# Kernel optimization log

Measured on AMD Instinct MI355X. Metric: run time of the kernel, lower is better.

## Reference

```python
import jax, jax.numpy as jnp
import numpy as np

N_NODES = 100000

def prelu(x, alpha):
    return jnp.where(x >= 0, x, alpha * x)

def setup_inputs() -> dict:
    key = jax.random.key(0)
    ks = jax.random.split(key, 8)
    N, E, D = N_NODES, 1600000, 128
    AX = jax.random.normal(ks[0], (N, D), dtype=jnp.float32)
    A_row = jax.random.randint(ks[1], (E,), 0, N, dtype=jnp.int32)
    A_col = jax.random.randint(ks[2], (E,), 0, N, dtype=jnp.int32)
    A_val = jax.random.uniform(ks[3], (E,), dtype=jnp.float32)
    # Xavier-uniform linear weights, zero bias (as in module init)
    lim = float(np.sqrt(6.0 / (D + D)))
    Wr_w = jax.random.uniform(ks[4], (D, D), minval=-lim, maxval=lim, dtype=jnp.float32)
    W_w = jax.random.uniform(ks[5], (D, D), minval=-lim, maxval=lim, dtype=jnp.float32)
    Wr_b = jnp.zeros((D,), dtype=jnp.float32)
    W_b = jnp.zeros((D,), dtype=jnp.float32)
    g_alpha = jnp.full((1,), 0.25, dtype=jnp.float32)    # PReLU default init
    act_alpha = jnp.full((1,), 0.25, dtype=jnp.float32)
    return {"AX": AX, "A_row": A_row, "A_col": A_col, "A_val": A_val,
            "Wr_w": Wr_w, "Wr_b": Wr_b, "W_w": W_w, "W_b": W_b,
            "g_alpha": g_alpha, "act_alpha": act_alpha}

def reference(AX, A_row, A_col, A_val, Wr_w, Wr_b, W_w, W_b, g_alpha, act_alpha):
    # h = g(Wr @ AX)  : [N, H]
    h = prelu(AX @ Wr_w.T + Wr_b, g_alpha)
    # SpMM: temp[i] = sum_{(i,j) in E} A_val * h[j]
    msgs = A_val[:, None] * h[A_col]                       # [E, H] gather
    temp = jax.ops.segment_sum(msgs, A_row, num_segments=N_NODES)
    # act(W @ temp), unsqueeze batch dim
    out = prelu(temp @ W_w.T + W_b, act_alpha)
    return out[None, :, :]
```

## Files before the change

kernel.cpp:

```cpp
#include <hip/hip_runtime.h>
#include <stdint.h>


typedef _Float16 half8 __attribute__((ext_vector_type(8)));
typedef _Float16 half4 __attribute__((ext_vector_type(4)));
typedef _Float16 half2v __attribute__((ext_vector_type(2)));
typedef float floatx4 __attribute__((ext_vector_type(4)));

#define LDK 136
#define SHIFT 5
#define NBMAX 3200
#define NBLK 256
#define SCT 1024
#define CAP 1024

__global__ __launch_bounds__(256, 3)
void gemm_hist(const float* __restrict__ X, const float* __restrict__ Wr,
               const float* __restrict__ bias, const float* __restrict__ alpha_p,
               _Float16* __restrict__ out, int N,
               const int* __restrict__ rows, int* __restrict__ hist_g,
               int E, int chunk, int NB,
               const float* __restrict__ W, _Float16* __restrict__ W16)
{
    __shared__ _Float16 Ws[128 * LDK];
    const int tid = threadIdx.x;

    if (blockIdx.x < NBLK) {
        const int hb = blockIdx.x;
        int* lh = (int*)Ws;
        if (hb == 0) {
#pragma unroll
            for (int j = 0; j < 64; ++j)
                W16[tid + j * 256] = (_Float16)W[tid + j * 256];
        }
        for (int i = tid; i < NB; i += 256) lh[i] = 0;
        __syncthreads();
        int s = hb * chunk, e = min(E, s + chunk);
        for (int i = s + tid; i < e; i += 256)
            atomicAdd(&lh[rows[i] >> SHIFT], 1);
        __syncthreads();
        for (int b = tid; b < NB; b += 256)
            hist_g[b * NBLK + hb] = lh[b];
        return;
    }

    const int bm  = (blockIdx.x - NBLK) * 128;
    const float alpha = *alpha_p;
    const int wave = tid >> 6;
    const int lane = tid & 63;
    const int l15  = lane & 15;
    const int quad = lane >> 4;

    half8 a[2][4];
#pragma unroll
    for (int mt = 0; mt < 2; ++mt) {
        const int xrow = bm + wave * 32 + mt * 16 + l15;
        const float* xp = X + (size_t)xrow * 128 + quad * 8;
        const bool ok = xrow < N;
#pragma unroll
        for (int k = 0; k < 4; ++k) {
            half8 hv = {};
            if (ok) {
                float4 f0 = *(const float4*)(xp + k * 32);
                float4 f1 = *(const float4*)(xp + k * 32 + 4);
                hv[0] = (_Float16)f0.x; hv[1] = (_Float16)f0.y;
                hv[2] = (_Float16)f0.z; hv[3] = (_Float16)f0.w;
                hv[4] = (_Float16)f1.x; hv[5] = (_Float16)f1.y;
                hv[6] = (_Float16)f1.z; hv[7] = (_Float16)f1.w;
            }
            a[mt][k] = hv;
        }
    }

#pragma unroll
    for (int i = 0; i < 16; ++i) {
        int c   = tid + i * 256;
        int row = c >> 5;
        int coff = (c & 31) * 4;
        float4 f = *(const float4*)(Wr + row * 128 + coff);
        half4 hv = { (_Float16)f.x, (_Float16)f.y, (_Float16)f.z, (_Float16)f.w };
        *(half4*)(&Ws[row * LDK + coff]) = hv;
    }
    __syncthreads();

    floatx4 acc[2][8] = {};
#pragma unroll
    for (int k = 0; k < 4; ++k) {
        const int k0 = k * 32;
        half8 b[8];
#pragma unroll
        for (int n = 0; n < 8; ++n)
            b[n] = *(const half8*)(&Ws[(n * 16 + l15) * LDK + k0 + quad * 8]);
#pragma unroll
        for (int n = 0; n < 8; ++n) {
            acc[0][n] = __builtin_amdgcn_mfma_f32_16x16x32_f16(a[0][k], b[n], acc[0][n], 0, 0, 0);
            acc[1][n] = __builtin_amdgcn_mfma_f32_16x16x32_f16(a[1][k], b[n], acc[1][n], 0, 0, 0);
        }
    }

#pragma unroll
    for (int mt = 0; mt < 2; ++mt) {
#pragma unroll
        for (int n = 0; n < 8; ++n) {
#pragma unroll
            for (int r = 0; r < 4; ++r) {
                int row = bm + wave * 32 + mt * 16 + quad * 4 + r;
                int col = n * 16 + l15;
                if (row < N) {
                    float v = acc[mt][n][r] + bias[col];
                    v = (v >= 0.f) ? v : alpha * v;
                    out[(size_t)row * 128 + col] = (_Float16)v;
                }
            }
        }
    }
}

__global__ __launch_bounds__(NBLK)
void bucket_scan1(int* __restrict__ hist_g, int* __restrict__ tot)
{
    __shared__ int sd[NBLK];
    int b = blockIdx.x, t = threadIdx.x;
    int v = hist_g[b * NBLK + t];
    sd[t] = v;
    __syncthreads();
    for (int off = 1; off < NBLK; off <<= 1) {
        int x = (t >= off) ? sd[t - off] : 0;
        __syncthreads();
        sd[t] += x;
        __syncthreads();
    }
    hist_g[b * NBLK + t] = sd[t] - v;
    if (t == NBLK - 1) tot[b] = sd[t];
}

__global__ __launch_bounds__(SCT)
void bucket_scatter(const int* __restrict__ rows, const int* __restrict__ cols,
                    const float* __restrict__ vals, const int* __restrict__ tot,
                    const int* __restrict__ hist_g, uint2* __restrict__ edges,
                    int* __restrict__ bkt_ptr, int E, int chunk, int NB)
{
    __shared__ int sd[SCT];
    __shared__ int cur[NBMAX];
    const int t = threadIdx.x, blk = blockIdx.x;

    int v[4]; int s = 0;
#pragma unroll
    for (int j = 0; j < 4; ++j) {
        int idx = t * 4 + j;
        v[j] = (idx < NB) ? tot[idx] : 0;
        s += v[j];
    }
    sd[t] = s;
    __syncthreads();
    for (int off = 1; off < SCT; off <<= 1) {
        int x = (t >= off) ? sd[t - off] : 0;
        __syncthreads();
        sd[t] += x;
        __syncthreads();
    }
    int base = (t == 0) ? 0 : sd[t - 1];
#pragma unroll
    for (int j = 0; j < 4; ++j) {
        int idx = t * 4 + j;
        if (idx < NB) {
            cur[idx] = base + hist_g[idx * NBLK + blk];
            if (blk == 0) bkt_ptr[idx] = base;
            base += v[j];
        }
    }
    if (blk == 0 && t == 0) bkt_ptr[NB] = E;
    __syncthreads();

    int s0 = blk * chunk, e0 = min(E, s0 + chunk);
    for (int i = s0 + t; i < e0; i += SCT) {
        int r = rows[i];
        int b = r >> SHIFT;
        uint2 ed;
        ed.x = (unsigned)cols[i] | ((unsigned)(r & 31) << 20);
        ed.y = __float_as_uint(vals[i]);
        int p = atomicAdd(&cur[b], 1);
        edges[p] = ed;
    }
}

__global__ __launch_bounds__(256, 8)
void spmm_fused(const int* __restrict__ bkt_ptr, const uint2* __restrict__ edges,
                const _Float16* __restrict__ h, const _Float16* __restrict__ W16,
                const float* __restrict__ bias, const float* __restrict__ alpha_p,
                float* __restrict__ out, int N)
{
    __shared__ uint2 eS[CAP];
    __shared__ _Float16 T[32 * LDK];
    __shared__ int bins[32], startS[33];

    const int tid  = threadIdx.x;
    const int wave = tid >> 6;
    const int lane = tid & 63;
    const int b    = blockIdx.x;
    const int s0   = bkt_ptr[b], e0 = bkt_ptr[b + 1];

    float acc[8][2] = {};

    for (int base = s0; base < e0; base += CAP) {
        const int n = min(CAP, e0 - base);
        if (tid < 32) bins[tid] = 0;
        __syncthreads();
        uint2 q[4];
#pragma unroll
        for (int u = 0; u < 4; ++u) {
            int i = tid + u * 256;
            if (i < n) {
                q[u] = edges[base + i];
                atomicAdd(&bins[q[u].x >> 20], 1);
            }
        }
        __syncthreads();
        if (tid < 32) {
            int x = bins[tid];
#pragma unroll
            for (int off = 1; off < 32; off <<= 1) {
                int y = __shfl_up(x, off);
                if (tid >= off) x += y;
            }
            startS[tid + 1] = x;
            if (tid == 0) startS[0] = 0;
            bins[tid] = x - bins[tid];
        }
        __syncthreads();
#pragma unroll
        for (int u = 0; u < 4; ++u) {
            int i = tid + u * 256;
            if (i < n) {
                int p = atomicAdd(&bins[q[u].x >> 20], 1);
                eS[p] = q[u];
            }
        }
        __syncthreads();

#pragma unroll
        for (int j = 0; j < 8; ++j) {
            int r  = wave * 8 + j;
            int rs = startS[r], re = startS[r + 1];
            float a0r = acc[j][0], a1r = acc[j][1];
            int i = rs;
            for (; i + 7 < re; i += 8) {
                uint2 q0 = eS[i],     q1 = eS[i + 1], q2 = eS[i + 2], q3 = eS[i + 3];
                uint2 q4 = eS[i + 4], q5 = eS[i + 5], q6 = eS[i + 6], q7 = eS[i + 7];
                half2v v0 = *(const half2v*)(h + (size_t)(q0.x & 0xFFFFF) * 128 + lane * 2);
                half2v v1 = *(const half2v*)(h + (size_t)(q1.x & 0xFFFFF) * 128 + lane * 2);
                half2v v2 = *(const half2v*)(h + (size_t)(q2.x & 0xFFFFF) * 128 + lane * 2);
                half2v v3 = *(const half2v*)(h + (size_t)(q3.x & 0xFFFFF) * 128 + lane * 2);
                half2v v4 = *(const half2v*)(h + (size_t)(q4.x & 0xFFFFF) * 128 + lane * 2);
                half2v v5 = *(const half2v*)(h + (size_t)(q5.x & 0xFFFFF) * 128 + lane * 2);
                half2v v6 = *(const half2v*)(h + (size_t)(q6.x & 0xFFFFF) * 128 + lane * 2);
                half2v v7 = *(const half2v*)(h + (size_t)(q7.x & 0xFFFFF) * 128 + lane * 2);
                float w0 = __uint_as_float(q0.y), w1 = __uint_as_float(q1.y);
                float w2 = __uint_as_float(q2.y), w3 = __uint_as_float(q3.y);
                float w4 = __uint_as_float(q4.y), w5 = __uint_as_float(q5.y);
                float w6 = __uint_as_float(q6.y), w7 = __uint_as_float(q7.y);
                a0r += w0 * (float)v0[0]; a1r += w0 * (float)v0[1];
                a0r += w1 * (float)v1[0]; a1r += w1 * (float)v1[1];
                a0r += w2 * (float)v2[0]; a1r += w2 * (float)v2[1];
                a0r += w3 * (float)v3[0]; a1r += w3 * (float)v3[1];
                a0r += w4 * (float)v4[0]; a1r += w4 * (float)v4[1];
                a0r += w5 * (float)v5[0]; a1r += w5 * (float)v5[1];
                a0r += w6 * (float)v6[0]; a1r += w6 * (float)v6[1];
                a0r += w7 * (float)v7[0]; a1r += w7 * (float)v7[1];
            }
            for (; i + 1 < re; i += 2) {
                uint2 q0 = eS[i], q1 = eS[i + 1];
                half2v v0 = *(const half2v*)(h + (size_t)(q0.x & 0xFFFFF) * 128 + lane * 2);
                half2v v1 = *(const half2v*)(h + (size_t)(q1.x & 0xFFFFF) * 128 + lane * 2);
                float w0 = __uint_as_float(q0.y), w1 = __uint_as_float(q1.y);
                a0r += w0 * (float)v0[0]; a1r += w0 * (float)v0[1];
                a0r += w1 * (float)v1[0]; a1r += w1 * (float)v1[1];
            }
            if (i < re) {
                uint2 q0 = eS[i];
                half2v v0 = *(const half2v*)(h + (size_t)(q0.x & 0xFFFFF) * 128 + lane * 2);
                float w0 = __uint_as_float(q0.y);
                a0r += w0 * (float)v0[0]; a1r += w0 * (float)v0[1];
            }
            acc[j][0] = a0r; acc[j][1] = a1r;
        }
        __syncthreads();
    }

#pragma unroll
    for (int j = 0; j < 8; ++j) {
        half2v o = { (_Float16)acc[j][0], (_Float16)acc[j][1] };
        *(half2v*)(&T[(wave * 8 + j) * LDK + lane * 2]) = o;
    }
    __syncthreads();

    const float alpha = *alpha_p;
    const int l15  = lane & 15;
    const int quad = lane >> 4;
    floatx4 c[2][2] = {};
#pragma unroll
    for (int k0 = 0; k0 < 128; k0 += 32) {
        half8 a0 = *(const half8*)(&T[(     l15) * LDK + k0 + quad * 8]);
        half8 a1 = *(const half8*)(&T[(16 + l15) * LDK + k0 + quad * 8]);
#pragma unroll
        for (int nt = 0; nt < 2; ++nt) {
            int nrow = (wave * 2 + nt) * 16 + l15;
            half8 bf = *(const half8*)(W16 + nrow * 128 + k0 + quad * 8);
            c[0][nt] = __builtin_amdgcn_mfma_f32_16x16x32_f16(a0, bf, c[0][nt], 0, 0, 0);
            c[1][nt] = __builtin_amdgcn_mfma_f32_16x16x32_f16(a1, bf, c[1][nt], 0, 0, 0);
        }
    }
    const int row0 = b << SHIFT;
#pragma unroll
    for (int mt = 0; mt < 2; ++mt) {
#pragma unroll
        for (int nt = 0; nt < 2; ++nt) {
            int col = (wave * 2 + nt) * 16 + l15;
            float bcol = bias[col];
#pragma unroll
            for (int r = 0; r < 4; ++r) {
                int row = row0 + mt * 16 + quad * 4 + r;
                if (row < N) {
                    float v = c[mt][nt][r] + bcol;
                    v = (v >= 0.f) ? v : alpha * v;
                    out[(size_t)row * 128 + col] = v;
                }
            }
        }
    }
}

static inline size_t align256(size_t x) { return (x + 255) & ~(size_t)255; }

extern "C" void kernel_launch(void* const* d_in, const int* in_sizes, int n_in,
                              void* d_out, int out_size, void* d_ws, size_t ws_size,
                              hipStream_t stream)
{
    const float* AX        = (const float*)d_in[0];
    const int*   A_row     = (const int*)  d_in[1];
    const int*   A_col     = (const int*)  d_in[2];
    const float* A_val     = (const float*)d_in[3];
    const float* Wr_w      = (const float*)d_in[4];
    const float* Wr_b      = (const float*)d_in[5];
    const float* W_w       = (const float*)d_in[6];
    const float* W_b       = (const float*)d_in[7];
    const float* g_alpha   = (const float*)d_in[8];
    const float* act_alpha = (const float*)d_in[9];

    const int N = in_sizes[0] / 128;
    const int E = in_sizes[1];
    const int NB = (N + 31) >> SHIFT;
    const int chunk = (E + NBLK - 1) / NBLK;

    char* ws = (char*)d_ws;
    size_t off = 0;
    _Float16* h       = (_Float16*)(ws + off); off += align256((size_t)N * 128 * 2);
    uint2*    edges   = (uint2*)   (ws + off); off += align256((size_t)E * 8);
    int*      hist_g  = (int*)     (ws + off); off += align256((size_t)NB * NBLK * 4);
    int*      tot     = (int*)     (ws + off); off += align256((size_t)NB * 4);
    int*      bkt_ptr = (int*)     (ws + off); off += align256((size_t)(NB + 1) * 4);
    _Float16* W16     = (_Float16*)(ws + off); off += align256((size_t)128 * 128 * 2);
    (void)ws_size; (void)n_in; (void)out_size;

    const int gemmB = (N + 127) / 128;

    gemm_hist<<<NBLK + gemmB, 256, 0, stream>>>(AX, Wr_w, Wr_b, g_alpha, h, N,
                                                A_row, hist_g, E, chunk, NB,
                                                W_w, W16);
    bucket_scan1<<<NB, NBLK, 0, stream>>>(hist_g, tot);
    bucket_scatter<<<NBLK, SCT, 0, stream>>>(A_row, A_col, A_val, tot, hist_g,
                                             edges, bkt_ptr, E, chunk, NB);
    spmm_fused<<<NB, 256, 0, stream>>>(bkt_ptr, edges, h, W16, W_b, act_alpha,
                                       (float*)d_out, N);
}
```

Baseline: 266.7 us.

## Fuse edge scatter with dense GEMM and use wave-shuffle bucket scan

The histogram moves into its own 1024-thread kernel. The edge scatter phase is merged into the same launch as the first dense GEMM, so the heavy scatter overlaps with the MFMA work instead of the lighter histogram. The per-bucket scan is rewritten as one wave per bucket using shuffle-up prefix sums, replacing a shared-memory scan with many barriers. GEMM blocks grow to 1024 threads, with each wave computing a 16x64 tile, which changes occupancy and register use.

```diff
diff --git a/kernel.cpp b/kernel.cpp
--- a/kernel.cpp
+++ b/kernel.cpp
@@ -14,33 +14,108 @@
 #define SCT 1024
 #define CAP 1024
 
-__global__ __launch_bounds__(256, 3)
-void gemm_hist(const float* __restrict__ X, const float* __restrict__ Wr,
-               const float* __restrict__ bias, const float* __restrict__ alpha_p,
-               _Float16* __restrict__ out, int N,
-               const int* __restrict__ rows, int* __restrict__ hist_g,
-               int E, int chunk, int NB,
-               const float* __restrict__ W, _Float16* __restrict__ W16)
+__global__ __launch_bounds__(SCT)
+void bucket_hist(const int* __restrict__ rows, int* __restrict__ hist_g,
+                 int E, int chunk, int NB,
+                 const float* __restrict__ W, _Float16* __restrict__ W16)
+{
+    __shared__ int lh[NBMAX];
+    int tid = threadIdx.x, blk = blockIdx.x;
+    if (blk == 0) {
+#pragma unroll
+        for (int j = 0; j < 16; ++j) W16[tid + j * 1024] = (_Float16)W[tid + j * 1024];
+    }
+    for (int i = tid; i < NB; i += SCT) lh[i] = 0;
+    __syncthreads();
+    int s = blk * chunk, e = min(E, s + chunk);
+    for (int i = s + tid; i < e; i += SCT)
+        atomicAdd(&lh[rows[i] >> SHIFT], 1);
+    __syncthreads();
+    for (int b = tid; b < NB; b += SCT)
+        hist_g[b * NBLK + blk] = lh[b];
+}
+
+__global__ __launch_bounds__(256)
+void scan1_fast(int* __restrict__ hist_g, int* __restrict__ tot, int NB)
+{
+    const int wave = threadIdx.x >> 6;
+    const int lane = threadIdx.x & 63;
+    const int b = blockIdx.x * 4 + wave;
+    if (b >= NB) return;
+
+    int* p = hist_g + b * NBLK + lane * 4;
+    int v0 = p[0], v1 = p[1], v2 = p[2], v3 = p[3];
+    int s = v0 + v1 + v2 + v3;
+
+    int x = s;
+#pragma unroll
+    for (int off = 1; off < 64; off <<= 1) {
+        int y = __shfl_up(x, off);
+        if (lane >= off) x += y;
+    }
+    int run = x - s;
+    p[0] = run; run += v0;
+    p[1] = run; run += v1;
+    p[2] = run; run += v2;
+    p[3] = run;
+    if (lane == 63) tot[b] = x;
+}
+
+__global__ __launch_bounds__(1024, 4)
+void scatter_gemm(const int* __restrict__ rows, const int* __restrict__ cols,
+                  const float* __restrict__ vals, const int* __restrict__ tot,
+                  const int* __restrict__ hist_g, uint2* __restrict__ edges,
+                  int* __restrict__ bkt_ptr, int E, int chunk, int NB,
+                  const float* __restrict__ X, const float* __restrict__ Wr,
+                  const float* __restrict__ bias, const float* __restrict__ alpha_p,
+                  _Float16* __restrict__ out, int N)
 {
     __shared__ _Float16 Ws[128 * LDK];
     const int tid = threadIdx.x;
 
     if (blockIdx.x < NBLK) {
-        const int hb = blockIdx.x;
-        int* lh = (int*)Ws;
-        if (hb == 0) {
-#pragma unroll
-            for (int j = 0; j < 64; ++j)
-                W16[tid + j * 256] = (_Float16)W[tid + j * 256];
-        }
-        for (int i = tid; i < NB; i += 256) lh[i] = 0;
-        __syncthreads();
-        int s = hb * chunk, e = min(E, s + chunk);
-        for (int i = s + tid; i < e; i += 256)
-            atomicAdd(&lh[rows[i] >> SHIFT], 1);
-        __syncthreads();
-        for (int b = tid; b < NB; b += 256)
-            hist_g[b * NBLK + hb] = lh[b];
+        int* sd  = (int*)Ws;
+        int* cur = (int*)Ws + SCT;
+        const int blk = blockIdx.x;
+
+        int v[4]; int s = 0;
+#pragma unroll
+        for (int j = 0; j < 4; ++j) {
+            int idx = tid * 4 + j;
+            v[j] = (idx < NB) ? tot[idx] : 0;
+            s += v[j];
+        }
+        sd[tid] = s;
+        __syncthreads();
+        for (int off = 1; off < SCT; off <<= 1) {
+            int x = (tid >= off) ? sd[tid - off] : 0;
+            __syncthreads();
+            sd[tid] += x;
+            __syncthreads();
+        }
+        int base = (tid == 0) ? 0 : sd[tid - 1];
+#pragma unroll
+        for (int j = 0; j < 4; ++j) {
+            int idx = tid * 4 + j;
+            if (idx < NB) {
+                cur[idx] = base + hist_g[idx * NBLK + blk];
+                if (blk == 0) bkt_ptr[idx] = base;
+                base += v[j];
+            }
+        }
+        if (blk == 0 && tid == 0) bkt_ptr[NB] = E;
+        __syncthreads();
+
+        int s0 = blk * chunk, e0 = min(E, s0 + chunk);
+        for (int i = s0 + tid; i < e0; i += SCT) {
+            int r = rows[i];
+            int b = r >> SHIFT;
+            uint2 ed;
+            ed.x = (unsigned)cols[i] | ((unsigned)(r & 31) << 20);
+            ed.y = __float_as_uint(vals[i]);
+            int p = atomicAdd(&cur[b], 1);
+            edges[p] = ed;
+        }
         return;
     }
 
@@ -50,13 +125,14 @@
     const int lane = tid & 63;
     const int l15  = lane & 15;
     const int quad = lane >> 4;
-
-    half8 a[2][4];
-#pragma unroll
-    for (int mt = 0; mt < 2; ++mt) {
-        const int xrow = bm + wave * 32 + mt * 16 + l15;
+    const int mt   = wave >> 1;
+    const int nh   = wave & 1;
+
+    half8 a[4];
+    {
+        const int xrow = bm + mt * 16 + l15;
+        const bool ok = xrow < N;
         const float* xp = X + (size_t)xrow * 128 + quad * 8;
-        const bool ok = xrow < N;
 #pragma unroll
         for (int k = 0; k < 4; ++k) {
             half8 hv = {};
@@ -68,13 +144,13 @@
                 hv[4] = (_Float16)f1.x; hv[5] = (_Float16)f1.y;
                 hv[6] = (_Float16)f1.z; hv[7] = (_Float16)f1.w;
             }
-            a[mt][k] = hv;
-        }
-    }
-
-#pragma unroll
-    for (int i = 0; i < 16; ++i) {
-        int c   = tid + i * 256;
+            a[k] = hv;
+        }
+    }
+
+#pragma unroll
+    for (int i = 0; i < 4; ++i) {
+        int c   = tid + i * 1024;
         int row = c >> 5;
         int coff = (c & 31) * 4;
         float4 f = *(const float4*)(Wr + row * 128 + coff);
@@ -83,104 +159,30 @@
     }
     __syncthreads();
 
-    floatx4 acc[2][8] = {};
+    floatx4 acc[4] = {};
 #pragma unroll
     for (int k = 0; k < 4; ++k) {
-        const int k0 = k * 32;
-        half8 b[8];
-#pragma unroll
-        for (int n = 0; n < 8; ++n)
-            b[n] = *(const half8*)(&Ws[(n * 16 + l15) * LDK + k0 + quad * 8]);
-#pragma unroll
-        for (int n = 0; n < 8; ++n) {
-            acc[0][n] = __builtin_amdgcn_mfma_f32_16x16x32_f16(a[0][k], b[n], acc[0][n], 0, 0, 0);
-            acc[1][n] = __builtin_amdgcn_mfma_f32_16x16x32_f16(a[1][k], b[n], acc[1][n], 0, 0, 0);
-        }
-    }
-
-#pragma unroll
-    for (int mt = 0; mt < 2; ++mt) {
-#pragma unroll
-        for (int n = 0; n < 8; ++n) {
-#pragma unroll
-            for (int r = 0; r < 4; ++r) {
-                int row = bm + wave * 32 + mt * 16 + quad * 4 + r;
-                int col = n * 16 + l15;
-                if (row < N) {
-                    float v = acc[mt][n][r] + bias[col];
-                    v = (v >= 0.f) ? v : alpha * v;
-                    out[(size_t)row * 128 + col] = (_Float16)v;
-                }
-            }
-        }
-    }
-}
-
-__global__ __launch_bounds__(NBLK)
-void bucket_scan1(int* __restrict__ hist_g, int* __restrict__ tot)
-{
-    __shared__ int sd[NBLK];
-    int b = blockIdx.x, t = threadIdx.x;
-    int v = hist_g[b * NBLK + t];
-    sd[t] = v;
-    __syncthreads();
-    for (int off = 1; off < NBLK; off <<= 1) {
-        int x = (t >= off) ? sd[t - off] : 0;
-        __syncthreads();
-        sd[t] += x;
-        __syncthreads();
-    }
-    hist_g[b * NBLK + t] = sd[t] - v;
-    if (t == NBLK - 1) tot[b] = sd[t];
-}
-
-__global__ __launch_bounds__(SCT)
-void bucket_scatter(const int* __restrict__ rows, const int* __restrict__ cols,
-                    const float* __restrict__ vals, const int* __restrict__ tot,
-                    const int* __restrict__ hist_g, uint2* __restrict__ edges,
-                    int* __restrict__ bkt_ptr, int E, int chunk, int NB)
-{
-    __shared__ int sd[SCT];
-    __shared__ int cur[NBMAX];
-    const int t = threadIdx.x, blk = blockIdx.x;
-
-    int v[4]; int s = 0;
-#pragma unroll
-    for (int j = 0; j < 4; ++j) {
-        int idx = t * 4 + j;
-        v[j] = (idx < NB) ? tot[idx] : 0;
-        s += v[j];
-    }
-    sd[t] = s;
-    __syncthreads();
-    for (int off = 1; off < SCT; off <<= 1) {
-        int x = (t >= off) ? sd[t - off] : 0;
-        __syncthreads();
-        sd[t] += x;
-        __syncthreads();
-    }
-    int base = (t == 0) ? 0 : sd[t - 1];
-#pragma unroll
-    for (int j = 0; j < 4; ++j) {
-        int idx = t * 4 + j;
-        if (idx < NB) {
-            cur[idx] = base + hist_g[idx * NBLK + blk];
-            if (blk == 0) bkt_ptr[idx] = base;
-            base += v[j];
-        }
-    }
-    if (blk == 0 && t == 0) bkt_ptr[NB] = E;
-    __syncthreads();
-
-    int s0 = blk * chunk, e0 = min(E, s0 + chunk);
-    for (int i = s0 + t; i < e0; i += SCT) {
-        int r = rows[i];
-        int b = r >> SHIFT;
-        uint2 ed;
-        ed.x = (unsigned)cols[i] | ((unsigned)(r & 31) << 20);
-        ed.y = __float_as_uint(vals[i]);
-        int p = atomicAdd(&cur[b], 1);
-        edges[p] = ed;
+#pragma unroll
+        for (int n = 0; n < 4; ++n) {
+            int nc = nh * 4 + n;
+            half8 b = *(const half8*)(&Ws[(nc * 16 + l15) * LDK + k * 32 + quad * 8]);
+            acc[n] = __builtin_amdgcn_mfma_f32_16x16x32_f16(a[k], b, acc[n], 0, 0, 0);
+        }
+    }
+
+#pragma unroll
+    for (int n = 0; n < 4; ++n) {
+        int col = (nh * 4 + n) * 16 + l15;
+        float bcol = bias[col];
+#pragma unroll
+        for (int r = 0; r < 4; ++r) {
+            int row = bm + mt * 16 + quad * 4 + r;
+            if (row < N) {
+                float v = acc[n][r] + bcol;
+                v = (v >= 0.f) ? v : alpha * v;
+                out[(size_t)row * 128 + col] = (_Float16)v;
+            }
+        }
     }
 }
 
@@ -364,12 +366,11 @@
 
     const int gemmB = (N + 127) / 128;
 
-    gemm_hist<<<NBLK + gemmB, 256, 0, stream>>>(AX, Wr_w, Wr_b, g_alpha, h, N,
-                                                A_row, hist_g, E, chunk, NB,
-                                                W_w, W16);
-    bucket_scan1<<<NB, NBLK, 0, stream>>>(hist_g, tot);
-    bucket_scatter<<<NBLK, SCT, 0, stream>>>(A_row, A_col, A_val, tot, hist_g,
-                                             edges, bkt_ptr, E, chunk, NB);
+    bucket_hist<<<NBLK, SCT, 0, stream>>>(A_row, hist_g, E, chunk, NB, W_w, W16);
+    scan1_fast<<<(NB + 3) / 4, 256, 0, stream>>>(hist_g, tot, NB);
+    scatter_gemm<<<NBLK + gemmB, 1024, 0, stream>>>(A_row, A_col, A_val, tot, hist_g,
+                                                    edges, bkt_ptr, E, chunk, NB,
+                                                    AX, Wr_w, Wr_b, g_alpha, h, N);
     spmm_fused<<<NB, 256, 0, stream>>>(bkt_ptr, edges, h, W16, W_b, act_alpha,
                                        (float*)d_out, N);
 }
```

Measured after the change: 250.2 us. -6.2%, faster.
